# Kernel optimization log

Measured on AMD Instinct MI355X. Metric: run time of the kernel, lower is better.

## Reference

```python
import jax, jax.numpy as jnp
import numpy as np

B, H, C, N, K_TERMS = 256, 512, 64, 100, 8


def eval_cubic_spline(coeffs, tobs, t):
    # coeffs: [B, N-1, 4, C]; tobs: [N] sorted knots; t: scalar
    idx = jnp.clip(jnp.searchsorted(tobs, t, side='right') - 1, 0, tobs.shape[0] - 2)
    dt = t - tobs[idx]
    c = coeffs[:, idx]  # [B, 4, C]
    # Horner evaluation: c0 + c1*dt + c2*dt^2 + c3*dt^3
    return c[:, 0] + dt * (c[:, 1] + dt * (c[:, 2] + dt * c[:, 3]))


def setup_inputs() -> dict:
    key = jax.random.key(0)
    k_h, k_c, k_dc, k_wx, k_wh, k_wo = jax.random.split(key, 6)
    xav = lambda k, shape: jax.random.uniform(
        k, shape, minval=-1.0, maxval=1.0, dtype=jnp.float32
    ) * np.float32(np.sqrt(6.0 / (shape[0] + shape[1])))
    return {
        't': jnp.float32(0.5),
        'h': jax.random.normal(k_h, (B, H), dtype=jnp.float32),
        'coeffs': jax.random.normal(k_c, (B, N - 1, 4, C), dtype=jnp.float32),
        'dcoeffs': jax.random.normal(k_dc, (B, N - 1, 4, C), dtype=jnp.float32),
        'tobs': jnp.linspace(0.0, 1.0, N, dtype=jnp.float32),
        'wx': xav(k_wx, (H, C)),
        'wh': xav(k_wh, (H, H)),
        'wout': xav(k_wo, (H, H)),
        'b0': jnp.zeros((H,), dtype=jnp.float32),
        'b1': jnp.zeros((H,), dtype=jnp.float32),
    }


def reference(t, h, coeffs, dcoeffs, tobs, wx, wh, wout, b0, b1):
    x = eval_cubic_spline(coeffs, tobs, t)      # [B, C]
    xdot = eval_cubic_spline(dcoeffs, tobs, t)  # [B, C]
    l1 = x @ wx.T + h @ wh.T + b0               # [B, H]
    relu = jnp.maximum(l1, 0.0)
    th = jnp.tanh(relu @ wout.T + b1)           # [B, H]
    dtanh = 1.0 - th * th
    drelu = jax.nn.sigmoid(l1)                  # surrogate_relu branch
    # Jacobian assembly via broadcasted outer product: [B, H, H]
    d_outer = dtanh[:, :, None] * wout[None, :, :] * drelu[:, None, :]
    Jx = d_outer @ wx                           # [B, H, C]
    Jh = d_outer @ wh                           # [B, H, H]
    curr = jnp.einsum('bhc,bc->bh', Jx, xdot)   # jx matvec, [B, H]
    h_dot = curr
    for _ in range(K_TERMS):                    # Neumann-series recurrence
        curr = jnp.einsum('bij,bj->bi', Jh, curr)
        h_dot = h_dot + curr
    return h_dot
```

## Files before the change

### kernel.cpp

```cpp
#include <hip/hip_runtime.h>

#define BB 256
#define HH 512
#define CC 64
#define NN 100
#define KT 8

typedef short s16x8 __attribute__((ext_vector_type(8)));
typedef float f32x4 __attribute__((ext_vector_type(4)));

#define MFMA16(a, b, c) __builtin_amdgcn_mfma_f32_16x16x32_bf16((a), (b), (c), 0, 0, 0)

static __device__ __forceinline__ unsigned short f2bf(float f) {
    union { float f; unsigned int u; } v; v.f = f;
    unsigned int r = v.u + 0x7FFFu + ((v.u >> 16) & 1u);
    return (unsigned short)(r >> 16);
}


__global__ void k_pack(const float* __restrict__ wh, const float* __restrict__ wout,
                       const float* __restrict__ wx, const float* __restrict__ h,
                       const float* __restrict__ coeffs, const float* __restrict__ dcoeffs,
                       const float* __restrict__ tobs, const float* __restrict__ tg,
                       unsigned short* __restrict__ whp, unsigned short* __restrict__ wop,
                       unsigned short* __restrict__ wxp, unsigned short* __restrict__ hb,
                       unsigned short* __restrict__ xb, unsigned short* __restrict__ xdb) {
    int gid = blockIdx.x * 256 + threadIdx.x;
    if (gid < 524288) {
        const float* src = (gid < 262144) ? wh : wout;
        unsigned short* dst = (gid < 262144) ? whp : wop;
        int p = gid & 262143;
        int e = p & 7, lane = (p >> 3) & 63, g = (p >> 9) & 15, cg = (p >> 13) & 1, w = p >> 14;
        int row = w * 32 + cg * 16 + (lane & 15);
        int k = g * 32 + (lane >> 4) * 8 + e;
        dst[p] = f2bf(src[row * HH + k]);
    } else if (gid < 557056) {
        int p = gid - 524288;
        int e = p & 7, lane = (p >> 3) & 63, g = (p >> 9) & 1, cg = (p >> 10) & 1, w = p >> 11;
        int row = w * 32 + cg * 16 + (lane & 15);
        int k = g * 32 + (lane >> 4) * 8 + e;
        wxp[p] = f2bf(wx[row * CC + k]);
    } else if (gid < 688128) {
        int p = gid - 557056;
        hb[p] = f2bf(h[p]);
    } else if (gid < 704512) {
        int p = gid - 688128;
        int b = p >> 6, c = p & 63;
        float t = tg[0];
        int cntv = 0;
        for (int n = 0; n < NN; n++) cntv += (tobs[n] <= t) ? 1 : 0;
        int idx = cntv - 1;
        idx = idx < 0 ? 0 : (idx > NN - 2 ? NN - 2 : idx);
        float dt = t - tobs[idx];
        const float* cb = coeffs + ((size_t)(b * (NN - 1) + idx) * 4) * CC + c;
        float xv = cb[0] + dt * (cb[CC] + dt * (cb[2 * CC] + dt * cb[3 * CC]));
        const float* db = dcoeffs + ((size_t)(b * (NN - 1) + idx) * 4) * CC + c;
        float xd = db[0] + dt * (db[CC] + dt * (db[2 * CC] + dt * db[3 * CC]));
        xb[p] = f2bf(xv);
        xdb[p] = f2bf(xd);
    }
}

__global__ void k_l1(const unsigned short* __restrict__ whp, const unsigned short* __restrict__ wxp,
                     const unsigned short* __restrict__ hb, const unsigned short* __restrict__ xb,
                     const unsigned short* __restrict__ xdb, const float* __restrict__ b0g,
                     unsigned short* __restrict__ relu_b, float* __restrict__ drelu_f,
                     unsigned short* __restrict__ s0_b) {
    __shared__ unsigned short sh[32][520];
    __shared__ unsigned short sx[32][72];
    __shared__ unsigned short sxd[32][72];
    int tid = threadIdx.x;
    int b0 = blockIdx.x * 32;
    int it = blockIdx.y;
    for (int idx = tid; idx < 32 * 64; idx += 256) {
        int r = idx >> 6, c8 = idx & 63;
        *(int4*)&sh[r][c8 * 8] = *(const int4*)&hb[(b0 + r) * HH + c8 * 8];
    }
    for (int idx = tid; idx < 32 * 8; idx += 256) {
        int r = idx >> 3, c8 = idx & 7;
        *(int4*)&sx[r][c8 * 8] = *(const int4*)&xb[(b0 + r) * CC + c8 * 8];
        *(int4*)&sxd[r][c8 * 8] = *(const int4*)&xdb[(b0 + r) * CC + c8 * 8];
    }
    __syncthreads();
    int wv = tid >> 6, lane = tid & 63, col = lane & 15, kq = lane >> 4;
    int isub = it * 64 + wv * 16;
    int wpk = isub >> 5, cg = (isub >> 4) & 1;
    f32x4 acc0 = {0.f, 0.f, 0.f, 0.f}, acc1 = {0.f, 0.f, 0.f, 0.f};
    f32x4 vac0 = {0.f, 0.f, 0.f, 0.f}, vac1 = {0.f, 0.f, 0.f, 0.f};
    const s16x8* whfrag = (const s16x8*)whp + (size_t)((wpk * 2 + cg) * 16) * 64 + lane;
#pragma unroll
    for (int g = 0; g < 16; g++) {
        s16x8 bf = whfrag[g * 64];
        s16x8 a0 = *(const s16x8*)&sh[col][g * 32 + kq * 8];
        s16x8 a1 = *(const s16x8*)&sh[16 + col][g * 32 + kq * 8];
        acc0 = MFMA16(a0, bf, acc0);
        acc1 = MFMA16(a1, bf, acc1);
    }
    const s16x8* wxfrag = (const s16x8*)wxp + (size_t)((wpk * 2 + cg) * 2) * 64 + lane;
#pragma unroll
    for (int g = 0; g < 2; g++) {
        s16x8 bf = wxfrag[g * 64];
        s16x8 a0 = *(const s16x8*)&sx[col][g * 32 + kq * 8];
        s16x8 a1 = *(const s16x8*)&sx[16 + col][g * 32 + kq * 8];
        acc0 = MFMA16(a0, bf, acc0);
        acc1 = MFMA16(a1, bf, acc1);
        s16x8 d0 = *(const s16x8*)&sxd[col][g * 32 + kq * 8];
        s16x8 d1 = *(const s16x8*)&sxd[16 + col][g * 32 + kq * 8];
        vac0 = MFMA16(d0, bf, vac0);
        vac1 = MFMA16(d1, bf, vac1);
    }
    int ic = isub + col;
    float bias = b0g[ic];
#pragma unroll
    for (int r = 0; r < 4; r++) {
        int bb = b0 + kq * 4 + r;
        float l1a = acc0[r] + bias;
        float dra = 1.f / (1.f + expf(-l1a));
        relu_b[bb * HH + ic] = f2bf(fmaxf(l1a, 0.f));
        drelu_f[bb * HH + ic] = dra;
        s0_b[bb * HH + ic] = f2bf(dra * vac0[r]);
        float l1b = acc1[r] + bias;
        float drb = 1.f / (1.f + expf(-l1b));
        relu_b[(bb + 16) * HH + ic] = f2bf(fmaxf(l1b, 0.f));
        drelu_f[(bb + 16) * HH + ic] = drb;
        s0_b[(bb + 16) * HH + ic] = f2bf(drb * vac1[r]);
    }
}

__global__ void k_th(const unsigned short* __restrict__ wop, const unsigned short* __restrict__ relu_b,
                     const unsigned short* __restrict__ s0_b, const float* __restrict__ b1g,
                     float* __restrict__ dtanh_f, unsigned short* __restrict__ curr_b,
                     float* __restrict__ curr0_f, unsigned int* __restrict__ flg) {
    __shared__ unsigned short sr[32][520];
    __shared__ unsigned short ss0[32][520];
    int tid = threadIdx.x;
    if (blockIdx.x == 0 && blockIdx.y == 0) {
        flg[tid] = 0u;
        flg[tid + 256] = 0u;
    }
    int b0 = blockIdx.x * 32;
    int it = blockIdx.y;
    for (int idx = tid; idx < 32 * 64; idx += 256) {
        int r = idx >> 6, c8 = idx & 63;
        *(int4*)&sr[r][c8 * 8] = *(const int4*)&relu_b[(b0 + r) * HH + c8 * 8];
        *(int4*)&ss0[r][c8 * 8] = *(const int4*)&s0_b[(b0 + r) * HH + c8 * 8];
    }
    __syncthreads();
    int wv = tid >> 6, lane = tid & 63, col = lane & 15, kq = lane >> 4;
    int isub = it * 64 + wv * 16;
    int wpk = isub >> 5, cg = (isub >> 4) & 1;
    f32x4 acc0 = {0.f, 0.f, 0.f, 0.f}, acc1 = {0.f, 0.f, 0.f, 0.f};
    f32x4 cac0 = {0.f, 0.f, 0.f, 0.f}, cac1 = {0.f, 0.f, 0.f, 0.f};
    const s16x8* wofrag = (const s16x8*)wop + (size_t)((wpk * 2 + cg) * 16) * 64 + lane;
#pragma unroll
    for (int g = 0; g < 16; g++) {
        s16x8 bf = wofrag[g * 64];
        s16x8 a0 = *(const s16x8*)&sr[col][g * 32 + kq * 8];
        s16x8 a1 = *(const s16x8*)&sr[16 + col][g * 32 + kq * 8];
        acc0 = MFMA16(a0, bf, acc0);
        acc1 = MFMA16(a1, bf, acc1);
        s16x8 p0 = *(const s16x8*)&ss0[col][g * 32 + kq * 8];
        s16x8 p1 = *(const s16x8*)&ss0[16 + col][g * 32 + kq * 8];
        cac0 = MFMA16(p0, bf, cac0);
        cac1 = MFMA16(p1, bf, cac1);
    }
    int ic = isub + col;
    float bias = b1g[ic];
    int fc = (ic >> 5) * 512 + (ic & 7) + (((ic >> 3) & 3) << 7);
#pragma unroll
    for (int r = 0; r < 4; r++) {
        int bb = b0 + kq * 4 + r;
        int row8 = (kq * 4 + r) * 8;
        float th_a = tanhf(acc0[r] + bias);
        float dta = 1.f - th_a * th_a;
        float c0a = dta * cac0[r];
        dtanh_f[bb * HH + ic] = dta;
        curr_b[(bb >> 4) * 8192 + fc + row8] = f2bf(c0a);
        curr0_f[bb * HH + ic] = c0a;
        float th_b = tanhf(acc1[r] + bias);
        float dtb = 1.f - th_b * th_b;
        float c0b = dtb * cac1[r];
        dtanh_f[(bb + 16) * HH + ic] = dtb;
        curr_b[((bb + 16) >> 4) * 8192 + fc + row8] = f2bf(c0b);
        curr0_f[(bb + 16) * HH + ic] = c0b;
    }
}

__global__ __launch_bounds__(512) void k_loop6(
    const unsigned short* __restrict__ whp, const unsigned short* __restrict__ wop,
    const unsigned short* __restrict__ curr_b, const float* __restrict__ curr0_f,
    const float* __restrict__ drelu_f, const float* __restrict__ dtanh_f,
    unsigned short* __restrict__ xch, unsigned int* flg,
    float* __restrict__ outp) {
    __shared__ __align__(16) unsigned short sa[2][8192];
    const int tid = threadIdx.x;
    const int w = tid >> 6, lane = tid & 63;
    const int col2 = lane & 15, kq = lane >> 4;
    const int c = blockIdx.x & 15;
    const int s = blockIdx.x >> 4;

    {
        const int4* src = (const int4*)(curr_b + (size_t)c * 8192);
        int4* dst = (int4*)&sa[0][0];
        dst[tid] = src[tid];
        dst[tid + 512] = src[tid + 512];
    }

    float dr[2][4], dt[2][4], hd[2][4];
#pragma unroll
    for (int t = 0; t < 2; t++) {
        const int cc = s * 256 + (w * 2 + t) * 16 + col2;
#pragma unroll
        for (int r = 0; r < 4; r++) {
            const int row = c * 16 + kq * 4 + r;
            dr[t][r] = drelu_f[row * HH + cc];
            dt[t][r] = dtanh_f[row * HH + cc];
            hd[t][r] = curr0_f[row * HH + cc];
        }
    }

    int fbl[2];
#pragma unroll
    for (int t = 0; t < 2; t++)
        fbl[t] = w * 512 + (col2 & 7) + (((t * 2 + (col2 >> 3)) & 3) << 7) + kq * 32;
    const int myhalf = s * 4096;
    const int phalf = (1 - s) * 4096;

    const s16x8* wlh = (const s16x8*)whp + (size_t)(s * 16 + w * 2) * 1024 + lane;
    const s16x8* wlo = (const s16x8*)wop + (size_t)(s * 16 + w * 2) * 1024 + lane;
    const unsigned short* A0 = &sa[0][lane * 8];
    const unsigned short* A1 = &sa[1][lane * 8];
    unsigned int* fme = flg + (s * 16 + c) * 16;
    unsigned int* fpr = flg + ((1 - s) * 16 + c) * 16;

    __syncthreads();

    for (int p = 0; p < 16; p++) {
        if (p) {
            if (tid == 0) {
                while (__hip_atomic_load(fpr, __ATOMIC_RELAXED, __HIP_MEMORY_SCOPE_AGENT)
                       < (unsigned)p) { __builtin_amdgcn_s_sleep(1); }
            }
            __syncthreads();
            const unsigned long long* gsrc = (const unsigned long long*)
                (xch + ((size_t)(c * 2 + ((p - 1) & 1)) * 2 + (1 - s)) * 4096);
            unsigned long long v0 = __hip_atomic_load(&gsrc[tid], __ATOMIC_RELAXED, __HIP_MEMORY_SCOPE_AGENT);
            unsigned long long v1 = __hip_atomic_load(&gsrc[tid + 512], __ATOMIC_RELAXED, __HIP_MEMORY_SCOPE_AGENT);
            unsigned long long* ld = (unsigned long long*)&sa[p & 1][phalf];
            ld[tid] = v0;
            ld[tid + 512] = v1;
            __syncthreads();
        }
        const s16x8* wl = (p & 1) ? wlo : wlh;
        const unsigned short* Ar = (p & 1) ? A1 : A0;
        f32x4 acc[2] = {{0.f, 0.f, 0.f, 0.f}, {0.f, 0.f, 0.f, 0.f}};
        s16x8 bfr[2][2];
#pragma unroll
        for (int t = 0; t < 2; t++) bfr[0][t] = wl[t * 1024];
#pragma unroll
        for (int g = 0; g < 16; g++) {
            if (g < 15) {
#pragma unroll
                for (int t = 0; t < 2; t++) bfr[(g + 1) & 1][t] = wl[t * 1024 + (g + 1) * 64];
            }
            const s16x8 a = *(const s16x8*)(Ar + (size_t)g * 512);
#pragma unroll
            for (int t = 0; t < 2; t++) acc[t] = MFMA16(a, bfr[g & 1][t], acc[t]);
        }
        unsigned short* Aw = &sa[(p + 1) & 1][0];
        if (p & 1) {
            if (p < 15) {
#pragma unroll
                for (int t = 0; t < 2; t++)
#pragma unroll
                    for (int r = 0; r < 4; r++) {
                        float v = dt[t][r] * acc[t][r];
                        hd[t][r] += v;
                        Aw[myhalf + fbl[t] + r * 8] = f2bf(v);
                    }
            } else {
#pragma unroll
                for (int t = 0; t < 2; t++)
#pragma unroll
                    for (int r = 0; r < 4; r++) hd[t][r] += dt[t][r] * acc[t][r];
            }
        } else {
#pragma unroll
            for (int t = 0; t < 2; t++)
#pragma unroll
                for (int r = 0; r < 4; r++)
                    Aw[myhalf + fbl[t] + r * 8] = f2bf(dr[t][r] * acc[t][r]);
        }
        if (p < 15) {
            __syncthreads();
            unsigned long long* gdst = (unsigned long long*)
                (xch + ((size_t)(c * 2 + (p & 1)) * 2 + s) * 4096);
            const unsigned long long* lsrc = (const unsigned long long*)&sa[(p + 1) & 1][myhalf];
            __hip_atomic_store(&gdst[tid], lsrc[tid], __ATOMIC_RELAXED, __HIP_MEMORY_SCOPE_AGENT);
            __hip_atomic_store(&gdst[tid + 512], lsrc[tid + 512], __ATOMIC_RELAXED, __HIP_MEMORY_SCOPE_AGENT);
            __syncthreads();
            if (tid == 0)
                __hip_atomic_store(fme, (unsigned)(p + 1), __ATOMIC_RELEASE, __HIP_MEMORY_SCOPE_AGENT);
        }
    }

#pragma unroll
    for (int t = 0; t < 2; t++) {
        const int cc = s * 256 + (w * 2 + t) * 16 + col2;
#pragma unroll
        for (int r = 0; r < 4; r++)
            outp[(size_t)(c * 16 + kq * 4 + r) * HH + cc] = hd[t][r];
    }
}

extern "C" void kernel_launch(void* const* d_in, const int* in_sizes, int n_in,
                              void* d_out, int out_size, void* d_ws, size_t ws_size,
                              hipStream_t stream) {
    const float* tg = (const float*)d_in[0];
    const float* h = (const float*)d_in[1];
    const float* coeffs = (const float*)d_in[2];
    const float* dcoeffs = (const float*)d_in[3];
    const float* tobs = (const float*)d_in[4];
    const float* wx = (const float*)d_in[5];
    const float* wh = (const float*)d_in[6];
    const float* wout = (const float*)d_in[7];
    const float* b0g = (const float*)d_in[8];
    const float* b1g = (const float*)d_in[9];
    float* outp = (float*)d_out;

    char* ws = (char*)d_ws;
    unsigned short* whp    = (unsigned short*)(ws + 0);
    unsigned short* wop    = (unsigned short*)(ws + 524288);
    unsigned short* wxp    = (unsigned short*)(ws + 1048576);
    unsigned short* hb     = (unsigned short*)(ws + 1114112);
    unsigned short* xb     = (unsigned short*)(ws + 1376256);
    unsigned short* xdb    = (unsigned short*)(ws + 1409024);
    unsigned short* relu_b = (unsigned short*)(ws + 1441792);
    unsigned short* s0_b   = (unsigned short*)(ws + 1703936);
    float* drelu_f         = (float*)(ws + 1966080);
    float* dtanh_f         = (float*)(ws + 2490368);
    unsigned short* curr_b = (unsigned short*)(ws + 3014656);
    float* curr0_f         = (float*)(ws + 3276800);
    unsigned short* xch    = (unsigned short*)(ws + 1441792);
    unsigned int* flg      = (unsigned int*)(ws + 3801088);

    k_pack<<<2752, 256, 0, stream>>>(wh, wout, wx, h, coeffs, dcoeffs, tobs, tg,
                                     whp, wop, wxp, hb, xb, xdb);
    k_l1<<<dim3(8, 8), 256, 0, stream>>>(whp, wxp, hb, xb, xdb, b0g, relu_b, drelu_f, s0_b);
    k_th<<<dim3(8, 8), 256, 0, stream>>>(wop, relu_b, s0_b, b1g, dtanh_f, curr_b, curr0_f, flg);
    k_loop6<<<32, 512, 0, stream>>>(whp, wop, curr_b, curr0_f, drelu_f, dtanh_f, xch, flg, outp);
}
```

Before: 171.1 us.

## Overlap partner-exchange wait with MFMA over the locally owned K half

Each loop iteration is split into two halves along the reduction dimension. The block first runs the MFMA products for the half of the current vector it produced itself, then waits on the partner block's flag and loads its exchanged half, then runs the remaining products. This is meant to hide the cross-block spin-wait and global exchange latency behind useful compute. The risk is in the weight-pointer offsets (sK/pK), which must line up with the packed K ordering, and in the extra live registers across the barrier.

```diff
diff --git a/kernel.cpp b/kernel.cpp
--- a/kernel.cpp
+++ b/kernel.cpp
@@ -186,7 +186,7 @@
     }
 }
 
-__global__ __launch_bounds__(512) void k_loop6(
+__global__ __launch_bounds__(512) void k_loop7(
     const unsigned short* __restrict__ whp, const unsigned short* __restrict__ wop,
     const unsigned short* __restrict__ curr_b, const float* __restrict__ curr0_f,
     const float* __restrict__ drelu_f, const float* __restrict__ dtanh_f,
@@ -232,10 +232,35 @@
     const unsigned short* A1 = &sa[1][lane * 8];
     unsigned int* fme = flg + (s * 16 + c) * 16;
     unsigned int* fpr = flg + ((1 - s) * 16 + c) * 16;
+    const int sK = s << 9;
+    const int pK = (1 - s) << 9;
 
     __syncthreads();
 
     for (int p = 0; p < 16; p++) {
+        const s16x8* wl = (p & 1) ? wlo : wlh;
+        const unsigned short* Ar = (p & 1) ? A1 : A0;
+        const s16x8* w1 = wl + sK;
+        const s16x8* w2 = wl + pK;
+        f32x4 acc[2] = {{0.f, 0.f, 0.f, 0.f}, {0.f, 0.f, 0.f, 0.f}};
+        s16x8 bfr[2][2];
+#pragma unroll
+        for (int t = 0; t < 2; t++) bfr[0][t] = w1[t * 1024];
+#pragma unroll
+        for (int j = 0; j < 7; j++) {
+#pragma unroll
+            for (int t = 0; t < 2; t++) bfr[(j + 1) & 1][t] = w1[t * 1024 + (j + 1) * 64];
+            const s16x8 a = *(const s16x8*)(Ar + myhalf + j * 512);
+#pragma unroll
+            for (int t = 0; t < 2; t++) acc[t] = MFMA16(a, bfr[j & 1][t], acc[t]);
+        }
+        {
+#pragma unroll
+            for (int t = 0; t < 2; t++) bfr[0][t] = w2[t * 1024];
+            const s16x8 a = *(const s16x8*)(Ar + myhalf + 7 * 512);
+#pragma unroll
+            for (int t = 0; t < 2; t++) acc[t] = MFMA16(a, bfr[1][t], acc[t]);
+        }
         if (p) {
             if (tid == 0) {
                 while (__hip_atomic_load(fpr, __ATOMIC_RELAXED, __HIP_MEMORY_SCOPE_AGENT)
@@ -251,21 +276,18 @@
             ld[tid + 512] = v1;
             __syncthreads();
         }
-        const s16x8* wl = (p & 1) ? wlo : wlh;
-        const unsigned short* Ar = (p & 1) ? A1 : A0;
-        f32x4 acc[2] = {{0.f, 0.f, 0.f, 0.f}, {0.f, 0.f, 0.f, 0.f}};
-        s16x8 bfr[2][2];
-#pragma unroll
-        for (int t = 0; t < 2; t++) bfr[0][t] = wl[t * 1024];
-#pragma unroll
-        for (int g = 0; g < 16; g++) {
-            if (g < 15) {
-#pragma unroll
-                for (int t = 0; t < 2; t++) bfr[(g + 1) & 1][t] = wl[t * 1024 + (g + 1) * 64];
-            }
-            const s16x8 a = *(const s16x8*)(Ar + (size_t)g * 512);
-#pragma unroll
-            for (int t = 0; t < 2; t++) acc[t] = MFMA16(a, bfr[g & 1][t], acc[t]);
+#pragma unroll
+        for (int j = 0; j < 7; j++) {
+#pragma unroll
+            for (int t = 0; t < 2; t++) bfr[(j + 1) & 1][t] = w2[t * 1024 + (j + 1) * 64];
+            const s16x8 a = *(const s16x8*)(Ar + phalf + j * 512);
+#pragma unroll
+            for (int t = 0; t < 2; t++) acc[t] = MFMA16(a, bfr[j & 1][t], acc[t]);
+        }
+        {
+            const s16x8 a = *(const s16x8*)(Ar + phalf + 7 * 512);
+#pragma unroll
+            for (int t = 0; t < 2; t++) acc[t] = MFMA16(a, bfr[1][t], acc[t]);
         }
         unsigned short* Aw = &sa[(p + 1) & 1][0];
         if (p & 1) {
@@ -348,5 +370,5 @@
                                      whp, wop, wxp, hb, xb, xdb);
     k_l1<<<dim3(8, 8), 256, 0, stream>>>(whp, wxp, hb, xb, xdb, b0g, relu_b, drelu_f, s0_b);
     k_th<<<dim3(8, 8), 256, 0, stream>>>(wop, relu_b, s0_b, b1g, dtanh_f, curr_b, curr0_f, flg);
-    k_loop6<<<32, 512, 0, stream>>>(whp, wop, curr_b, curr0_f, drelu_f, dtanh_f, xch, flg, outp);
-}
+    k_loop7<<<32, 512, 0, stream>>>(whp, wop, curr_b, curr0_f, drelu_f, dtanh_f, xch, flg, outp);
+}
```

New measurement: 173.6 us. No clear change (+1.5%).

## Split Neumann loop across four blocks per batch tile with overlapped exchange

Applied to the files above, without the earlier changes.

The iterative Jacobian loop kernel now splits each 16-row batch tile's 512 output columns across four cooperating blocks instead of two, launching 64 blocks. Each wave computes one 16-column tile. It preloads all weight fragments and starts the MFMA chain on its locally owned K-slice while the peer slices are fetched from global memory after polling peer flags. Each thread packs its results into a 64-bit word and stores it directly, replacing the LDS round-trip and one barrier. This trades more parallelism and latency hiding for more cross-block flag polling, and it needs more flag words cleared.

```diff
diff --git a/kernel.cpp b/kernel.cpp
--- a/kernel.cpp
+++ b/kernel.cpp
@@ -137,6 +137,8 @@
     if (blockIdx.x == 0 && blockIdx.y == 0) {
         flg[tid] = 0u;
         flg[tid + 256] = 0u;
+        flg[tid + 512] = 0u;
+        flg[tid + 768] = 0u;
     }
     int b0 = blockIdx.x * 32;
     int it = blockIdx.y;
@@ -186,7 +188,7 @@
     }
 }
 
-__global__ __launch_bounds__(512) void k_loop6(
+__global__ __launch_bounds__(512) void k_loop10(
     const unsigned short* __restrict__ whp, const unsigned short* __restrict__ wop,
     const unsigned short* __restrict__ curr_b, const float* __restrict__ curr0_f,
     const float* __restrict__ drelu_f, const float* __restrict__ dtanh_f,
@@ -197,7 +199,7 @@
     const int w = tid >> 6, lane = tid & 63;
     const int col2 = lane & 15, kq = lane >> 4;
     const int c = blockIdx.x & 15;
-    const int s = blockIdx.x >> 4;
+    const int q = blockIdx.x >> 4;
 
     {
         const int4* src = (const int4*)(curr_b + (size_t)c * 8192);
@@ -206,111 +208,117 @@
         dst[tid + 512] = src[tid + 512];
     }
 
-    float dr[2][4], dt[2][4], hd[2][4];
-#pragma unroll
-    for (int t = 0; t < 2; t++) {
-        const int cc = s * 256 + (w * 2 + t) * 16 + col2;
-#pragma unroll
-        for (int r = 0; r < 4; r++) {
-            const int row = c * 16 + kq * 4 + r;
-            dr[t][r] = drelu_f[row * HH + cc];
-            dt[t][r] = dtanh_f[row * HH + cc];
-            hd[t][r] = curr0_f[row * HH + cc];
-        }
-    }
-
-    int fbl[2];
-#pragma unroll
-    for (int t = 0; t < 2; t++)
-        fbl[t] = w * 512 + (col2 & 7) + (((t * 2 + (col2 >> 3)) & 3) << 7) + kq * 32;
-    const int myhalf = s * 4096;
-    const int phalf = (1 - s) * 4096;
-
-    const s16x8* wlh = (const s16x8*)whp + (size_t)(s * 16 + w * 2) * 1024 + lane;
-    const s16x8* wlo = (const s16x8*)wop + (size_t)(s * 16 + w * 2) * 1024 + lane;
+    const int cc = (q * 8 + w) * 16 + col2;
+    float dr[4], dt[4], hd[4];
+#pragma unroll
+    for (int r = 0; r < 4; r++) {
+        const int row = c * 16 + kq * 4 + r;
+        dr[r] = drelu_f[row * HH + cc];
+        dt[r] = dtanh_f[row * HH + cc];
+        hd[r] = curr0_f[row * HH + cc];
+    }
+
+    const int fcom = (w >> 1) * 512 + (col2 & 7) + (((w * 2 + (col2 >> 3)) & 3) << 7) + kq * 32;
+    int fblq[4];
+#pragma unroll
+    for (int j = 0; j < 4; j++) fblq[j] = j * 2048 + fcom;
+    const int fb_own = q * 2048 + fcom;
+
+    const s16x8* wlh = (const s16x8*)whp + (size_t)(q * 8 + w) * 1024 + lane;
+    const s16x8* wlo = (const s16x8*)wop + (size_t)(q * 8 + w) * 1024 + lane;
     const unsigned short* A0 = &sa[0][lane * 8];
     const unsigned short* A1 = &sa[1][lane * 8];
-    unsigned int* fme = flg + (s * 16 + c) * 16;
-    unsigned int* fpr = flg + ((1 - s) * 16 + c) * 16;
+    unsigned int* fme = flg + (q * 16 + c) * 16;
 
     __syncthreads();
 
     for (int p = 0; p < 16; p++) {
-        if (p) {
-            if (tid == 0) {
-                while (__hip_atomic_load(fpr, __ATOMIC_RELAXED, __HIP_MEMORY_SCOPE_AGENT)
-                       < (unsigned)p) { __builtin_amdgcn_s_sleep(1); }
-            }
-            __syncthreads();
-            const unsigned long long* gsrc = (const unsigned long long*)
-                (xch + ((size_t)(c * 2 + ((p - 1) & 1)) * 2 + (1 - s)) * 4096);
-            unsigned long long v0 = __hip_atomic_load(&gsrc[tid], __ATOMIC_RELAXED, __HIP_MEMORY_SCOPE_AGENT);
-            unsigned long long v1 = __hip_atomic_load(&gsrc[tid + 512], __ATOMIC_RELAXED, __HIP_MEMORY_SCOPE_AGENT);
-            unsigned long long* ld = (unsigned long long*)&sa[p & 1][phalf];
-            ld[tid] = v0;
-            ld[tid + 512] = v1;
-            __syncthreads();
-        }
         const s16x8* wl = (p & 1) ? wlo : wlh;
         const unsigned short* Ar = (p & 1) ? A1 : A0;
-        f32x4 acc[2] = {{0.f, 0.f, 0.f, 0.f}, {0.f, 0.f, 0.f, 0.f}};
-        s16x8 bfr[2][2];
-#pragma unroll
-        for (int t = 0; t < 2; t++) bfr[0][t] = wl[t * 1024];
-#pragma unroll
-        for (int g = 0; g < 16; g++) {
-            if (g < 15) {
-#pragma unroll
-                for (int t = 0; t < 2; t++) bfr[(g + 1) & 1][t] = wl[t * 1024 + (g + 1) * 64];
+
+        s16x8 bfr[16];
+#pragma unroll
+        for (int d = 0; d < 16; d++) bfr[d] = wl[(((q << 2) + d) & 15) * 64];
+
+        unsigned long long v[4] = {0ull, 0ull, 0ull, 0ull};
+        if (p) {
+#pragma unroll
+            for (int j = 0; j < 4; j++) {
+                if (j != q) {
+                    const unsigned int* fj = flg + (j * 16 + c) * 16;
+                    while (__hip_atomic_load(fj, __ATOMIC_RELAXED, __HIP_MEMORY_SCOPE_AGENT)
+                           < (unsigned)p) { __builtin_amdgcn_s_sleep(1); }
+                }
             }
-            const s16x8 a = *(const s16x8*)(Ar + (size_t)g * 512);
-#pragma unroll
-            for (int t = 0; t < 2; t++) acc[t] = MFMA16(a, bfr[g & 1][t], acc[t]);
+#pragma unroll
+            for (int j = 0; j < 4; j++) {
+                if (j != q) {
+                    const unsigned long long* gsrc = (const unsigned long long*)(void*)xch
+                        + ((size_t)(c * 2 + ((p - 1) & 1)) * 4 + j) * 512;
+                    v[j] = __hip_atomic_load(&gsrc[tid], __ATOMIC_RELAXED, __HIP_MEMORY_SCOPE_AGENT);
+                }
+            }
+        }
+
+        f32x4 acc = {0.f, 0.f, 0.f, 0.f};
+#pragma unroll
+        for (int j = 0; j < 4; j++) {
+            const s16x8 a = *(const s16x8*)(Ar + q * 2048 + j * 512);
+            acc = MFMA16(a, bfr[j], acc);
+        }
+        if (p) {
+            unsigned short* ph = &sa[p & 1][0];
+#pragma unroll
+            for (int j = 0; j < 4; j++) {
+                if (j != q) {
+#pragma unroll
+                    for (int r = 0; r < 4; r++)
+                        ph[fblq[j] + r * 8] = (unsigned short)(v[j] >> (16 * r));
+                }
+            }
+        }
+        __syncthreads();
+#pragma unroll
+        for (int j = 4; j < 16; j++) {
+            const int go = (((q << 2) + j) & 15) * 512;
+            const s16x8 a = *(const s16x8*)(Ar + go);
+            acc = MFMA16(a, bfr[j], acc);
         }
         unsigned short* Aw = &sa[(p + 1) & 1][0];
-        if (p & 1) {
-            if (p < 15) {
-#pragma unroll
-                for (int t = 0; t < 2; t++)
-#pragma unroll
-                    for (int r = 0; r < 4; r++) {
-                        float v = dt[t][r] * acc[t][r];
-                        hd[t][r] += v;
-                        Aw[myhalf + fbl[t] + r * 8] = f2bf(v);
-                    }
+        if (p < 15) {
+            unsigned long long pk = 0ull;
+            if (p & 1) {
+#pragma unroll
+                for (int r = 0; r < 4; r++) {
+                    const float vv = dt[r] * acc[r];
+                    hd[r] += vv;
+                    const unsigned short b = f2bf(vv);
+                    Aw[fb_own + r * 8] = b;
+                    pk |= (unsigned long long)b << (16 * r);
+                }
             } else {
 #pragma unroll
-                for (int t = 0; t < 2; t++)
-#pragma unroll
-                    for (int r = 0; r < 4; r++) hd[t][r] += dt[t][r] * acc[t][r];
+                for (int r = 0; r < 4; r++) {
+                    const unsigned short b = f2bf(dr[r] * acc[r]);
+                    Aw[fb_own + r * 8] = b;
+                    pk |= (unsigned long long)b << (16 * r);
+                }
             }
-        } else {
-#pragma unroll
-            for (int t = 0; t < 2; t++)
-#pragma unroll
-                for (int r = 0; r < 4; r++)
-                    Aw[myhalf + fbl[t] + r * 8] = f2bf(dr[t][r] * acc[t][r]);
-        }
-        if (p < 15) {
-            __syncthreads();
-            unsigned long long* gdst = (unsigned long long*)
-                (xch + ((size_t)(c * 2 + (p & 1)) * 2 + s) * 4096);
-            const unsigned long long* lsrc = (const unsigned long long*)&sa[(p + 1) & 1][myhalf];
-            __hip_atomic_store(&gdst[tid], lsrc[tid], __ATOMIC_RELAXED, __HIP_MEMORY_SCOPE_AGENT);
-            __hip_atomic_store(&gdst[tid + 512], lsrc[tid + 512], __ATOMIC_RELAXED, __HIP_MEMORY_SCOPE_AGENT);
+            unsigned long long* gdst = (unsigned long long*)(void*)xch
+                + ((size_t)(c * 2 + (p & 1)) * 4 + q) * 512;
+            __hip_atomic_store(&gdst[tid], pk, __ATOMIC_RELAXED, __HIP_MEMORY_SCOPE_AGENT);
             __syncthreads();
             if (tid == 0)
                 __hip_atomic_store(fme, (unsigned)(p + 1), __ATOMIC_RELEASE, __HIP_MEMORY_SCOPE_AGENT);
-        }
-    }
-
-#pragma unroll
-    for (int t = 0; t < 2; t++) {
-        const int cc = s * 256 + (w * 2 + t) * 16 + col2;
-#pragma unroll
-        for (int r = 0; r < 4; r++)
-            outp[(size_t)(c * 16 + kq * 4 + r) * HH + cc] = hd[t][r];
-    }
+        } else {
+#pragma unroll
+            for (int r = 0; r < 4; r++) hd[r] += dt[r] * acc[r];
+        }
+    }
+
+#pragma unroll
+    for (int r = 0; r < 4; r++)
+        outp[(size_t)(c * 16 + kq * 4 + r) * HH + cc] = hd[r];
 }
 
 extern "C" void kernel_launch(void* const* d_in, const int* in_sizes, int n_in,
@@ -348,5 +356,5 @@
                                      whp, wop, wxp, hb, xb, xdb);
     k_l1<<<dim3(8, 8), 256, 0, stream>>>(whp, wxp, hb, xb, xdb, b0g, relu_b, drelu_f, s0_b);
     k_th<<<dim3(8, 8), 256, 0, stream>>>(wop, relu_b, s0_b, b1g, dtanh_f, curr_b, curr0_f, flg);
-    k_loop6<<<32, 512, 0, stream>>>(whp, wop, curr_b, curr0_f, drelu_f, dtanh_f, xch, flg, outp);
-}
+    k_loop10<<<64, 512, 0, stream>>>(whp, wop, curr_b, curr0_f, drelu_f, dtanh_f, xch, flg, outp);
+}
```

Result: faster. 161.6 us (-5.5%).
